# Performance work log

Measured on AMD Instinct MI355X. Metric: run time of the kernel, lower is better.

Reference implementation:

```python
import jax, jax.numpy as jnp
import numpy as np

EPS = 1e-5

def _offset_conv(x, w, b):
    # 3x3 conv, padding=1, producing 2*K*K offset channels (standard DeformConv2D v1)
    out = jax.lax.conv_general_dilated(x, w, (1, 1), ((1, 1), (1, 1)),
                                       dimension_numbers=('NCHW', 'OIHW', 'NCHW'))
    return out + b[None, :, None, None]

def _bilinear_gather(x, py, px):
    # x: [B,C,H,W]; py,px: [B,K2,H,W] float sample coords -> [B,C,K2,H,W]
    B, C, H, W = x.shape
    py = jnp.clip(py, 0.0, H - 1.0)
    px = jnp.clip(px, 0.0, W - 1.0)
    y0 = jnp.floor(py)
    x0 = jnp.floor(px)
    wy = py - y0
    wx = px - x0
    y0i = y0.astype(jnp.int32)
    x0i = x0.astype(jnp.int32)
    y1i = jnp.minimum(y0i + 1, H - 1)
    x1i = jnp.minimum(x0i + 1, W - 1)
    xf = x.reshape(B, C, H * W)
    K2, Ho, Wo = py.shape[1], py.shape[2], py.shape[3]
    def gather(yy, xx):
        idx = (yy * W + xx).reshape(B, 1, -1)  # broadcast over C
        return jnp.take_along_axis(xf, idx, axis=2).reshape(B, C, K2, Ho, Wo)
    v00 = gather(y0i, x0i)
    v01 = gather(y0i, x1i)
    v10 = gather(y1i, x0i)
    v11 = gather(y1i, x1i)
    wy = wy[:, None]
    wx = wx[:, None]
    return (v00 * (1 - wy) * (1 - wx) + v01 * (1 - wy) * wx
            + v10 * wy * (1 - wx) + v11 * wy * wx)

def _deform_dw(x, w_off, b_off, w_dw, k):
    # depthwise deformable conv, kernel k, padding k//2 (same spatial size)
    B, C, H, W = x.shape
    K2 = k * k
    off = _offset_conv(x, w_off, b_off)      # [B, 2*K2, H, W]
    dy, dx = off[:, :K2], off[:, K2:]
    r = (k - 1) // 2
    pn = jnp.arange(-r, r + 1, dtype=x.dtype)
    pn_y = jnp.repeat(pn, k)[None, :, None, None]  # [1,K2,1,1]
    pn_x = jnp.tile(pn, k)[None, :, None, None]
    gy = jnp.arange(H, dtype=x.dtype)[None, None, :, None]
    gx = jnp.arange(W, dtype=x.dtype)[None, None, None, :]
    py = gy + pn_y + dy
    px = gx + pn_x + dx
    samp = _bilinear_gather(x, py, px)        # [B,C,K2,H,W]
    return jnp.einsum('bckhw,ck->bchw', samp, w_dw.reshape(C, K2))

def _bn_relu(x, g, b, m, v):
    inv = g / jnp.sqrt(v + EPS)
    return jax.nn.relu(x * inv[None, :, None, None] + (b - m * inv)[None, :, None, None])

def setup_inputs() -> dict:
    key = jax.random.key(0)
    B, C, H, W, O = 4, 96, 64, 64, 192
    ks = jax.random.split(key, 32)
    d = {'x': jax.random.normal(ks[0], (B, C, H, W), jnp.float32)}
    i = 1
    for k in (3, 5, 7):
        K2 = k * k
        d[f'w_off{k}'] = 0.01 * jax.random.normal(ks[i], (2 * K2, C, 3, 3), jnp.float32); i += 1
        d[f'b_off{k}'] = jnp.zeros((2 * K2,), jnp.float32)
        d[f'w_dw{k}'] = jax.random.normal(ks[i], (C, k, k), jnp.float32) / k; i += 1
        d[f'g{k}'] = jnp.ones((C,), jnp.float32)
        d[f'be{k}'] = jnp.zeros((C,), jnp.float32)
        d[f'm{k}'] = 0.1 * jax.random.normal(ks[i], (C,), jnp.float32); i += 1
        d[f'v{k}'] = jax.random.uniform(ks[i], (C,), jnp.float32, 0.5, 1.5); i += 1
    d['w_pw'] = jax.random.normal(ks[i], (O, 3 * C), jnp.float32) / np.sqrt(3 * C).astype(np.float32); i += 1
    d['gp'] = jnp.ones((O,), jnp.float32)
    d['bp'] = jnp.zeros((O,), jnp.float32)
    d['mp'] = 0.1 * jax.random.normal(ks[i], (O,), jnp.float32); i += 1
    d['vp'] = jax.random.uniform(ks[i], (O,), jnp.float32, 0.5, 1.5)
    return d

def reference(x, w_off3, b_off3, w_dw3, g3, be3, m3, v3,
              w_off5, b_off5, w_dw5, g5, be5, m5, v5,
              w_off7, b_off7, w_dw7, g7, be7, m7, v7,
              w_pw, gp, bp, mp, vp):
    x1 = _bn_relu(_deform_dw(x, w_off3, b_off3, w_dw3, 3), g3, be3, m3, v3)
    x2 = _bn_relu(_deform_dw(x, w_off5, b_off5, w_dw5, 5), g5, be5, m5, v5)
    x3 = _bn_relu(_deform_dw(x, w_off7, b_off7, w_dw7, 7), g7, be7, m7, v7)
    xc = jnp.concatenate([x1, x2, x3], axis=1)  # [B, 3C, H, W]
    out = jnp.einsum('bchw,oc->bohw', xc, w_pw)  # 1x1 conv
    return _bn_relu(out, gp, bp, mp, vp)
```

## Files before the change

kernel.cpp:

```cpp
#include <hip/hip_runtime.h>
#include <hip/hip_fp16.h>
#include <math.h>

typedef unsigned short u16;
typedef _Float16 f16x8 __attribute__((ext_vector_type(8)));
typedef float f32x4 __attribute__((ext_vector_type(4)));

#define HWp 4096
#define Cc 96
#define Bb 4
#define Oo 192
#define C3 288

#define OFF_OFF   0
#define OFF_WDWT  3145728
#define OFF_BCAT  3159840
#define OFF_SBR   3160032
#define OFF_HBR   3160320
#define OFF_SPW   3160608
#define OFF_HPW   3160800
#define FP32_END  3160992
#define BF_XTPAD  0
#define BF_WOF    1672704
#define BF_WPW    1838592
#define BF_YT     1893888

__device__ __forceinline__ u16 f2h(float f) { return __half_as_ushort(__float2half(f)); }
__device__ __forceinline__ unsigned h2u(__half2 h) { union { __half2 h; unsigned u; } t; t.h = h; return t.u; }
__device__ __forceinline__ __half2 u2h(unsigned u) { union { __half2 h; unsigned u; } t; t.u = u; return t.h; }

#define PREP_N (165888 + 55296 + 14112 + 192 + 288 + 288 + 192 + 192 + 24960)
#define PREP_BLK ((PREP_N + 255) / 256)

__global__ __launch_bounds__(256) void prep_kernel(
    const float* __restrict__ x,
    const float* __restrict__ w3, const float* __restrict__ b3, const float* __restrict__ dw3,
    const float* __restrict__ g3, const float* __restrict__ be3, const float* __restrict__ m3, const float* __restrict__ v3,
    const float* __restrict__ w5, const float* __restrict__ b5, const float* __restrict__ dw5,
    const float* __restrict__ g5, const float* __restrict__ be5, const float* __restrict__ m5, const float* __restrict__ v5,
    const float* __restrict__ w7, const float* __restrict__ b7, const float* __restrict__ dw7,
    const float* __restrict__ g7, const float* __restrict__ be7, const float* __restrict__ m7, const float* __restrict__ v7,
    const float* __restrict__ wpw,
    const float* __restrict__ gp, const float* __restrict__ bp, const float* __restrict__ mp, const float* __restrict__ vp,
    float* __restrict__ ws)
{
    __shared__ u16 sT[64 * 104];
    u16* bf = (u16*)(ws + FP32_END);
    const int tid = threadIdx.x;

    if (blockIdx.x < 256) {
        const int b = blockIdx.x >> 6, h = blockIdx.x & 63;
        const float* xb = x + (((size_t)b * Cc) << 12) + (h << 6);
#pragma unroll
        for (int it = 0; it < 24; ++it) {
            int j = tid + it * 256;
            int c = j >> 6, p = j & 63;
            sT[p * 104 + c] = f2h(xb[((size_t)c << 12) + p]);
        }
        __syncthreads();
        u16* dst = bf + BF_XTPAD + ((size_t)(b * 66 + h + 1) * 66 + 1) * 96;
#pragma unroll
        for (int it = 0; it < 6; ++it) {
            int j = tid + it * 256;
            int pos = j / 24, c4 = j % 24;
            const u16* s = &sT[pos * 104 + c4 * 4];
            *(uint2*)(dst + pos * 96 + c4 * 4) = make_uint2(
                (unsigned)s[0] | ((unsigned)s[1] << 16),
                (unsigned)s[2] | ((unsigned)s[3] << 16));
        }
        return;
    }

    int i = (blockIdx.x - 256) * 256 + tid;
    if (i < 165888) {
        int f = i / 13824, r = i % 13824;
        int s = r >> 9, l = r & 511;
        int lane = l >> 3, j = l & 7;
        int o = f * 16 + (lane & 15);
        int k = s * 32 + (lane >> 4) * 8 + j;
        int tap = k / 96, c = k % 96;
        float v = 0.f;
        if (o < 18)       v = w3[o * 864 + c * 9 + tap];
        else if (o < 68)  v = w5[(o - 18) * 864 + c * 9 + tap];
        else if (o < 166) v = w7[(o - 68) * 864 + c * 9 + tap];
        bf[BF_WOF + i] = f2h(v);
        return;
    }
    int j = i - 165888;
    if (j < 55296) {
        int f = j / 4608, r = j % 4608;
        int s = r >> 9, l = r & 511;
        int lane = l >> 3, jj = l & 7;
        int o = f * 16 + (lane & 15);
        int k = s * 32 + (lane >> 4) * 8 + jj;
        bf[BF_WPW + j] = f2h(wpw[o * C3 + k]);
        return;
    }
    j -= 55296;
    if (j < 14112) {
        int ksel = j / 4704, rem = j % 4704;
        int t = rem / 96, c = rem % 96;
        int K2 = (ksel == 0) ? 9 : (ksel == 1) ? 25 : 49;
        const float* dw = (ksel == 0) ? dw3 : (ksel == 1) ? dw5 : dw7;
        ws[OFF_WDWT + j] = (t < K2) ? dw[c * K2 + t] : 0.f;
        return;
    }
    j -= 14112;
    if (j < 192) {
        float v = 0.f;
        if (j < 18)       v = b3[j];
        else if (j < 68)  v = b5[j - 18];
        else if (j < 166) v = b7[j - 68];
        ws[OFF_BCAT + j] = v;
        return;
    }
    j -= 192;
    if (j < C3) {
        int ks = j / Cc, c = j % Cc;
        const float* g = (ks == 0) ? g3 : (ks == 1) ? g5 : g7;
        const float* v = (ks == 0) ? v3 : (ks == 1) ? v5 : v7;
        ws[OFF_SBR + j] = g[c] / sqrtf(v[c] + 1e-5f);
        return;
    }
    j -= C3;
    if (j < C3) {
        int ks = j / Cc, c = j % Cc;
        const float* g = (ks == 0) ? g3 : (ks == 1) ? g5 : g7;
        const float* v = (ks == 0) ? v3 : (ks == 1) ? v5 : v7;
        const float* be = (ks == 0) ? be3 : (ks == 1) ? be5 : be7;
        const float* m = (ks == 0) ? m3 : (ks == 1) ? m5 : m7;
        float inv = g[c] / sqrtf(v[c] + 1e-5f);
        ws[OFF_HBR + j] = be[c] - m[c] * inv;
        return;
    }
    j -= C3;
    if (j < Oo) { ws[OFF_SPW + j] = gp[j] / sqrtf(vp[j] + 1e-5f); return; }
    j -= Oo;
    if (j < Oo) {
        float inv = gp[j] / sqrtf(vp[j] + 1e-5f);
        ws[OFF_HPW + j] = bp[j] - mp[j] * inv;
        return;
    }
    j -= Oo;
    if (j < 24960) {
        int c4 = j % 24, rem = j / 24;
        int cell = rem % 260, bb = rem / 260;
        int row, col;
        if (cell < 66)       { row = 0;  col = cell; }
        else if (cell < 132) { row = 65; col = cell - 66; }
        else if (cell < 196) { row = cell - 132 + 1; col = 0; }
        else                 { row = cell - 196 + 1; col = 65; }
        u16* dst = bf + BF_XTPAD + ((size_t)(bb * 66 + row) * 66 + col) * 96 + c4 * 4;
        *(uint2*)dst = make_uint2(0u, 0u);
        return;
    }
}

__global__ __launch_bounds__(512) void offconv_mfma(
    const float* __restrict__ ws, float* __restrict__ off)
{
    __shared__ u16 sX[3 * 66 * 98];
    const u16* bf = (const u16*)(ws + FP32_END);
    const u16* xp = bf + BF_XTPAD;
    const u16* wof = bf + BF_WOF;
    const int tid = threadIdx.x;
    const int lane = tid & 63, wid = tid >> 6;
    const int lane15 = lane & 15, quad = lane >> 4;
    const int h = blockIdx.x;
    const int b = blockIdx.z;
    const int f0 = (wid >> 2) * 6;
    const int pos = (wid & 3) * 16 + lane15;

#pragma unroll
    for (int it = 0; it < 10; ++it) {
        int j = tid + it * 512;
        if (j < 4752) {
            int r = j / (66 * 24);
            int rem = j % (66 * 24);
            int col = rem / 24, c4 = rem % 24;
            uint2 v = *(const uint2*)(xp + ((size_t)((b * 66 + h + r) * 66 + col)) * 96 + c4 * 4);
            *(uint2*)(&sX[(r * 66 + col) * 98 + c4 * 4]) = v;
        }
    }
    __syncthreads();

    f32x4 acc[6];
#pragma unroll
    for (int f = 0; f < 6; ++f) acc[f] = (f32x4){0.f, 0.f, 0.f, 0.f};

#pragma unroll
    for (int tap = 0; tap < 9; ++tap) {
        const int ky = tap / 3, kx = tap % 3;
        const u16* brow = &sX[(ky * 66 + kx + pos) * 98 + quad * 8];
#pragma unroll
        for (int cc = 0; cc < 3; ++cc) {
            f16x8 bb = *(const f16x8*)(brow + cc * 32);
            const int s = tap * 3 + cc;
#pragma unroll
            for (int f = 0; f < 6; ++f) {
                f16x8 a = *(const f16x8*)(wof + ((size_t)((f0 + f) * 27 + s) * 64 + lane) * 8);
                acc[f] = __builtin_amdgcn_mfma_f32_16x16x32_f16(a, bb, acc[f], 0, 0, 0);
            }
        }
    }

    const float* bcat = ws + OFF_BCAT;
    const int p = (h << 6) + pos;
#pragma unroll
    for (int f = 0; f < 6; ++f) {
        float* dst = off + (((size_t)(b * 192 + (f0 + f) * 16 + quad * 4)) << 12) + p;
#pragma unroll
        for (int r = 0; r < 4; ++r)
            dst[(size_t)r << 12] = acc[f][r] + bcat[(f0 + f) * 16 + quad * 4 + r];
    }
}

template<int K>
__device__ __forceinline__ void samp_v7(
    int ksel, int p0, int rounds, uint4* __restrict__ sWI,
    const float* __restrict__ ws, u16* __restrict__ yt)
{
    constexpr int K2 = K * K;
    constexpr int R = (K - 1) / 2;
    const int tb = (ksel == 0) ? 0 : ((ksel == 1) ? 18 : 68);

    const int tid = threadIdx.x;
    const int b = blockIdx.z;
    const float* offb = ws + OFF_OFF + ((size_t)(b * 192 + tb)) * HWp;
    const int c8 = tid % 12;
    const int q  = tid / 12;
    const int c = c8 * 8;
    const u16* xh = (const u16*)(ws + FP32_END) + BF_XTPAD + (size_t)b * 66 * 66 * 96;
    const char* xcb = (const char*)xh + c * 2;
    const float* wdT = ws + OFF_WDWT + ksel * 4704 + c;

    for (int r = 0; r < rounds; ++r) {
        const int p0r = p0 + r * 20;
        for (int i = tid; i < K2 * 20; i += 256) {
            int t = i / 20, qq = i % 20;
            int p = min(p0r + qq, 4095);
            int hh = p >> 6, wp = p & 63;
            float dy = offb[(size_t)t * HWp + p];
            float dx = offb[(size_t)(K2 + t) * HWp + p];
            int ky = t / K - R, kx = t % K - R;
            float py = fminf(fmaxf((float)(hh + ky) + dy, 0.f), 63.f);
            float px = fminf(fmaxf((float)(wp + kx) + dx, 0.f), 63.f);
            float fy = floorf(py), fx = floorf(px);
            int y0 = (int)fy, x0 = (int)fx;
            float wy = py - fy, wx = px - fx;
            int y1 = min(y0 + 1, 63), x1 = min(x0 + 1, 63);
            float w11 = wy * wx;
            float w10 = wy - w11;
            float w01 = wx - w11;
            float w00 = 1.f - wy - wx + w11;
            unsigned wA = h2u(__floats2half2_rn(w00, w01));
            unsigned wB = h2u(__floats2half2_rn(w10, w11));
            unsigned o00 = (unsigned)((y0 + 1) * 66 + (x0 + 1)) * 192u;
            unsigned d01 = (unsigned)(x1 - x0) * 192u;
            unsigned d10 = (unsigned)(y1 - y0) * 12672u;
            sWI[i] = make_uint4(wA, wB, o00, d01 | (d10 << 16));
        }
        __syncthreads();

        const int p = p0r + q;
        if (tid < 240 && p < 4096) {
            float acc[8];
#pragma unroll
            for (int k = 0; k < 8; ++k) acc[k] = 0.f;

            for (int t = 0; t < K2; ++t) {
                const uint4 e = sWI[t * 20 + q];
                const __half2 wA = u2h(e.x), wB = u2h(e.y);
                const __half2 w00b = __low2half2(wA), w01b = __high2half2(wA);
                const __half2 w10b = __low2half2(wB), w11b = __high2half2(wB);
                const unsigned d01 = e.w & 0xffffu, d10 = e.w >> 16;
                const uint4 u00 = *(const uint4*)(xcb + e.z);
                const uint4 u01 = *(const uint4*)(xcb + e.z + d01);
                const uint4 u10 = *(const uint4*)(xcb + e.z + d10);
                const uint4 u11 = *(const uint4*)(xcb + e.z + d10 + d01);
                const float4 wda = *(const float4*)(wdT + t * 96);
                const float4 wdb = *(const float4*)(wdT + t * 96 + 4);
                const unsigned a00[4] = {u00.x, u00.y, u00.z, u00.w};
                const unsigned a01[4] = {u01.x, u01.y, u01.z, u01.w};
                const unsigned a10[4] = {u10.x, u10.y, u10.z, u10.w};
                const unsigned a11[4] = {u11.x, u11.y, u11.z, u11.w};
                const float wd[8] = {wda.x, wda.y, wda.z, wda.w, wdb.x, wdb.y, wdb.z, wdb.w};
#pragma unroll
                for (int d = 0; d < 4; ++d) {
                    __half2 v = __hmul2(w00b, u2h(a00[d]));
                    v = __hfma2(w01b, u2h(a01[d]), v);
                    v = __hfma2(w10b, u2h(a10[d]), v);
                    v = __hfma2(w11b, u2h(a11[d]), v);
                    acc[2 * d]     = fmaf(wd[2 * d],     __low2float(v),  acc[2 * d]);
                    acc[2 * d + 1] = fmaf(wd[2 * d + 1], __high2float(v), acc[2 * d + 1]);
                }
            }

            const int cb = ksel * Cc + c;
            const float4 sa = *(const float4*)(ws + OFF_SBR + cb);
            const float4 sb = *(const float4*)(ws + OFF_SBR + cb + 4);
            const float4 ha = *(const float4*)(ws + OFF_HBR + cb);
            const float4 hb = *(const float4*)(ws + OFF_HBR + cb + 4);
            const float ss[8] = {sa.x, sa.y, sa.z, sa.w, sb.x, sb.y, sb.z, sb.w};
            const float hh8[8] = {ha.x, ha.y, ha.z, ha.w, hb.x, hb.y, hb.z, hb.w};
            unsigned rr[4];
#pragma unroll
            for (int d = 0; d < 4; ++d) {
                float lo = fmaxf(fmaf(acc[2 * d],     ss[2 * d],     hh8[2 * d]),     0.f);
                float hi = fmaxf(fmaf(acc[2 * d + 1], ss[2 * d + 1], hh8[2 * d + 1]), 0.f);
                rr[d] = h2u(__floats2half2_rn(lo, hi));
            }
            *(uint4*)(yt + ((size_t)(b << 12) + p) * C3 + cb) = make_uint4(rr[0], rr[1], rr[2], rr[3]);
        }
        if (r + 1 < rounds) __syncthreads();
    }
}

__global__ __launch_bounds__(256, 6) void sampdw7_kernel(float* __restrict__ ws)
{
    __shared__ uint4 sWI[980];
    u16* yt = (u16*)(ws + FP32_END) + BF_YT;
    const int bx = blockIdx.x;
    if (bx < 41)        samp_v7<3>(0, bx * 100, 5, sWI, ws, yt);
    else if (bx < 144)  samp_v7<5>(1, (bx - 41) * 40, 2, sWI, ws, yt);
    else                samp_v7<7>(2, (bx - 144) * 20, 1, sWI, ws, yt);
}

__global__ __launch_bounds__(512) void pwconv_mfma(
    const float* __restrict__ ws, float* __restrict__ out)
{
    __shared__ u16 sB[64 * 296];
    const u16* bf = (const u16*)(ws + FP32_END);
    const u16* yt = bf + BF_YT;
    const u16* wpw = bf + BF_WPW;
    const int tid = threadIdx.x;
    const int lane = tid & 63, wid = tid >> 6;
    const int lane15 = lane & 15, quad = lane >> 4;
    const int p0 = blockIdx.x * 64;
    const int b = blockIdx.z;
    const int f0 = (wid >> 2) * 6;
    const int pos = (wid & 3) * 16 + lane15;

#pragma unroll
    for (int it = 0; it < 5; ++it) {
        int j = tid + it * 512;
        if (j < 2304) {
            int ps = j / 36, c8 = j % 36;
            *(uint4*)(&sB[ps * 296 + c8 * 8]) =
                *(const uint4*)(yt + ((size_t)(b << 12) + p0 + ps) * C3 + c8 * 8);
        }
    }
    __syncthreads();

    f32x4 acc[6];
#pragma unroll
    for (int f = 0; f < 6; ++f) acc[f] = (f32x4){0.f, 0.f, 0.f, 0.f};

    const u16* brow = &sB[pos * 296 + quad * 8];
#pragma unroll
    for (int s = 0; s < 9; ++s) {
        f16x8 bb = *(const f16x8*)(brow + s * 32);
#pragma unroll
        for (int f = 0; f < 6; ++f) {
            f16x8 a = *(const f16x8*)(wpw + ((size_t)((f0 + f) * 9 + s) * 64 + lane) * 8);
            acc[f] = __builtin_amdgcn_mfma_f32_16x16x32_f16(a, bb, acc[f], 0, 0, 0);
        }
    }

    const float* spw = ws + OFF_SPW;
    const float* hpw = ws + OFF_HPW;
    const int p = p0 + pos;
#pragma unroll
    for (int f = 0; f < 6; ++f) {
        float* dst = out + (((size_t)(b * Oo + (f0 + f) * 16 + quad * 4)) << 12) + p;
#pragma unroll
        for (int r = 0; r < 4; ++r) {
            int o = (f0 + f) * 16 + quad * 4 + r;
            dst[(size_t)r << 12] = fmaxf(fmaf(acc[f][r], spw[o], hpw[o]), 0.f);
        }
    }
}

extern "C" void kernel_launch(void* const* d_in, const int* in_sizes, int n_in,
                              void* d_out, int out_size, void* d_ws, size_t ws_size,
                              hipStream_t stream)
{
    const float* x     = (const float*)d_in[0];
    const float* w3    = (const float*)d_in[1];
    const float* b3    = (const float*)d_in[2];
    const float* dw3   = (const float*)d_in[3];
    const float* g3    = (const float*)d_in[4];
    const float* be3   = (const float*)d_in[5];
    const float* m3    = (const float*)d_in[6];
    const float* v3    = (const float*)d_in[7];
    const float* w5    = (const float*)d_in[8];
    const float* b5    = (const float*)d_in[9];
    const float* dw5   = (const float*)d_in[10];
    const float* g5    = (const float*)d_in[11];
    const float* be5   = (const float*)d_in[12];
    const float* m5    = (const float*)d_in[13];
    const float* v5    = (const float*)d_in[14];
    const float* w7    = (const float*)d_in[15];
    const float* b7    = (const float*)d_in[16];
    const float* dw7   = (const float*)d_in[17];
    const float* g7    = (const float*)d_in[18];
    const float* be7   = (const float*)d_in[19];
    const float* m7    = (const float*)d_in[20];
    const float* v7    = (const float*)d_in[21];
    const float* wpw   = (const float*)d_in[22];
    const float* gp    = (const float*)d_in[23];
    const float* bp    = (const float*)d_in[24];
    const float* mp    = (const float*)d_in[25];
    const float* vp    = (const float*)d_in[26];

    float* ws = (float*)d_ws;
    float* out = (float*)d_out;

    {
        prep_kernel<<<256 + PREP_BLK, 256, 0, stream>>>(
            x,
            w3, b3, dw3, g3, be3, m3, v3,
            w5, b5, dw5, g5, be5, m5, v5,
            w7, b7, dw7, g7, be7, m7, v7,
            wpw, gp, bp, mp, vp, ws);
    }
    {
        dim3 grid(64, 1, Bb);
        offconv_mfma<<<grid, 512, 0, stream>>>(ws, ws + OFF_OFF);
    }
    {
        dim3 grid(349, 1, Bb);
        sampdw7_kernel<<<grid, 256, 0, stream>>>(ws);
    }
    {
        dim3 grid(64, 1, Bb);
        pwconv_mfma<<<grid, 512, 0, stream>>>(ws, out);
    }
}
```

Before: 191.0 us.

## Fuse offset conv, deformable sampling and pointwise conv into one kernel

Replaces the three kernels (offset conv, deformable depthwise sampling, pointwise conv) with a single kernel that processes 16-pixel tiles. Offsets and the per-tile sampled activations stay in shared memory instead of being written to and re-read from global workspace. This removes two launches and the global traffic for the offset and intermediate tensors. In exchange, each block repeats the weight loads for a small tile, and only 192 of 256 threads are active during sampling, which may reduce parallelism per block.

```diff
diff --git a/kernel.cpp b/kernel.cpp
--- a/kernel.cpp
+++ b/kernel.cpp
@@ -12,18 +12,16 @@
 #define Oo 192
 #define C3 288
 
-#define OFF_OFF   0
-#define OFF_WDWT  3145728
-#define OFF_BCAT  3159840
-#define OFF_SBR   3160032
-#define OFF_HBR   3160320
-#define OFF_SPW   3160608
-#define OFF_HPW   3160800
-#define FP32_END  3160992
+#define OFF_WDWT  0
+#define OFF_BCAT  14112
+#define OFF_SBR   14304
+#define OFF_HBR   14592
+#define OFF_SPW   14880
+#define OFF_HPW   15072
+#define FP32_END  15264
 #define BF_XTPAD  0
 #define BF_WOF    1672704
 #define BF_WPW    1838592
-#define BF_YT     1893888
 
 __device__ __forceinline__ u16 f2h(float f) { return __half_as_ushort(__float2half(f)); }
 __device__ __forceinline__ unsigned h2u(__half2 h) { union { __half2 h; unsigned u; } t; t.h = h; return t.u; }
@@ -156,130 +154,127 @@
     }
 }
 
-__global__ __launch_bounds__(512) void offconv_mfma(
-    const float* __restrict__ ws, float* __restrict__ off)
+__global__ __launch_bounds__(256, 4) void mega_kernel(
+    const float* __restrict__ ws, float* __restrict__ out)
 {
-    __shared__ u16 sX[3 * 66 * 98];
+    __shared__ uint4 regA[1328];
+    __shared__ float regB[3072];
+    u16* sX = (u16*)regA;
+    uint4* sWI = regA;
+    float* soff = regB;
+    u16* ytile = (u16*)regB;
+
     const u16* bf = (const u16*)(ws + FP32_END);
     const u16* xp = bf + BF_XTPAD;
-    const u16* wof = bf + BF_WOF;
     const int tid = threadIdx.x;
     const int lane = tid & 63, wid = tid >> 6;
     const int lane15 = lane & 15, quad = lane >> 4;
-    const int h = blockIdx.x;
     const int b = blockIdx.z;
-    const int f0 = (wid >> 2) * 6;
-    const int pos = (wid & 3) * 16 + lane15;
-
-#pragma unroll
-    for (int it = 0; it < 10; ++it) {
-        int j = tid + it * 512;
-        if (j < 4752) {
-            int r = j / (66 * 24);
-            int rem = j % (66 * 24);
+    const int p0 = blockIdx.x * 16;
+    const int h = p0 >> 6;
+    const int w0 = p0 & 63;
+
+    {
+        const u16* src = xp + ((size_t)(b * 66 + h) * 66 + w0) * 96;
+        for (int j = tid; j < 1296; j += 256) {
+            int r = j / 432;
+            int rem = j % 432;
             int col = rem / 24, c4 = rem % 24;
-            uint2 v = *(const uint2*)(xp + ((size_t)((b * 66 + h + r) * 66 + col)) * 96 + c4 * 4);
-            *(uint2*)(&sX[(r * 66 + col) * 98 + c4 * 4]) = v;
+            uint2 v = *(const uint2*)(src + ((size_t)(r * 66 + col)) * 96 + c4 * 4);
+            *(uint2*)(&sX[(r * 18 + col) * 104 + c4 * 4]) = v;
         }
     }
     __syncthreads();
 
-    f32x4 acc[6];
-#pragma unroll
-    for (int f = 0; f < 6; ++f) acc[f] = (f32x4){0.f, 0.f, 0.f, 0.f};
-
-#pragma unroll
-    for (int tap = 0; tap < 9; ++tap) {
-        const int ky = tap / 3, kx = tap % 3;
-        const u16* brow = &sX[(ky * 66 + kx + pos) * 98 + quad * 8];
-#pragma unroll
-        for (int cc = 0; cc < 3; ++cc) {
-            f16x8 bb = *(const f16x8*)(brow + cc * 32);
-            const int s = tap * 3 + cc;
-#pragma unroll
-            for (int f = 0; f < 6; ++f) {
-                f16x8 a = *(const f16x8*)(wof + ((size_t)((f0 + f) * 27 + s) * 64 + lane) * 8);
-                acc[f] = __builtin_amdgcn_mfma_f32_16x16x32_f16(a, bb, acc[f], 0, 0, 0);
-            }
-        }
-    }
-
-    const float* bcat = ws + OFF_BCAT;
-    const int p = (h << 6) + pos;
-#pragma unroll
-    for (int f = 0; f < 6; ++f) {
-        float* dst = off + (((size_t)(b * 192 + (f0 + f) * 16 + quad * 4)) << 12) + p;
-#pragma unroll
-        for (int r = 0; r < 4; ++r)
-            dst[(size_t)r << 12] = acc[f][r] + bcat[(f0 + f) * 16 + quad * 4 + r];
-    }
-}
-
-template<int K>
-__device__ __forceinline__ void samp_v7(
-    int ksel, int p0, int rounds, uint4* __restrict__ sWI,
-    const float* __restrict__ ws, u16* __restrict__ yt)
-{
-    constexpr int K2 = K * K;
-    constexpr int R = (K - 1) / 2;
-    const int tb = (ksel == 0) ? 0 : ((ksel == 1) ? 18 : 68);
-
-    const int tid = threadIdx.x;
-    const int b = blockIdx.z;
-    const float* offb = ws + OFF_OFF + ((size_t)(b * 192 + tb)) * HWp;
-    const int c8 = tid % 12;
-    const int q  = tid / 12;
-    const int c = c8 * 8;
-    const u16* xh = (const u16*)(ws + FP32_END) + BF_XTPAD + (size_t)b * 66 * 66 * 96;
-    const char* xcb = (const char*)xh + c * 2;
-    const float* wdT = ws + OFF_WDWT + ksel * 4704 + c;
-
-    for (int r = 0; r < rounds; ++r) {
-        const int p0r = p0 + r * 20;
-        for (int i = tid; i < K2 * 20; i += 256) {
-            int t = i / 20, qq = i % 20;
-            int p = min(p0r + qq, 4095);
-            int hh = p >> 6, wp = p & 63;
-            float dy = offb[(size_t)t * HWp + p];
-            float dx = offb[(size_t)(K2 + t) * HWp + p];
-            int ky = t / K - R, kx = t % K - R;
-            float py = fminf(fmaxf((float)(hh + ky) + dy, 0.f), 63.f);
-            float px = fminf(fmaxf((float)(wp + kx) + dx, 0.f), 63.f);
-            float fy = floorf(py), fx = floorf(px);
-            int y0 = (int)fy, x0 = (int)fx;
-            float wy = py - fy, wx = px - fx;
-            int y1 = min(y0 + 1, 63), x1 = min(x0 + 1, 63);
-            float w11 = wy * wx;
-            float w10 = wy - w11;
-            float w01 = wx - w11;
-            float w00 = 1.f - wy - wx + w11;
-            unsigned wA = h2u(__floats2half2_rn(w00, w01));
-            unsigned wB = h2u(__floats2half2_rn(w10, w11));
-            unsigned o00 = (unsigned)((y0 + 1) * 66 + (x0 + 1)) * 192u;
-            unsigned d01 = (unsigned)(x1 - x0) * 192u;
-            unsigned d10 = (unsigned)(y1 - y0) * 12672u;
-            sWI[i] = make_uint4(wA, wB, o00, d01 | (d10 << 16));
-        }
-        __syncthreads();
-
-        const int p = p0r + q;
-        if (tid < 240 && p < 4096) {
+    {
+        const u16* wof = bf + BF_WOF;
+        f32x4 acc[3];
+#pragma unroll
+        for (int ff = 0; ff < 3; ++ff) acc[ff] = (f32x4){0.f, 0.f, 0.f, 0.f};
+#pragma unroll
+        for (int tap = 0; tap < 9; ++tap) {
+            const int ky2 = tap / 3, kx2 = tap % 3;
+            const u16* brow = &sX[(ky2 * 18 + kx2 + lane15) * 104 + quad * 8];
+#pragma unroll
+            for (int cc = 0; cc < 3; ++cc) {
+                f16x8 bb = *(const f16x8*)(brow + cc * 32);
+                const int s = tap * 3 + cc;
+#pragma unroll
+                for (int ff = 0; ff < 3; ++ff) {
+                    const int f = wid * 3 + ff;
+                    f16x8 a = *(const f16x8*)(wof + ((size_t)(f * 27 + s) * 64 + lane) * 8);
+                    acc[ff] = __builtin_amdgcn_mfma_f32_16x16x32_f16(a, bb, acc[ff], 0, 0, 0);
+                }
+            }
+        }
+        const float* bcat = ws + OFF_BCAT;
+#pragma unroll
+        for (int ff = 0; ff < 3; ++ff) {
+#pragma unroll
+            for (int r = 0; r < 4; ++r) {
+                int co = (wid * 3 + ff) * 16 + quad * 4 + r;
+                soff[co * 16 + lane15] = acc[ff][r] + bcat[co];
+            }
+        }
+    }
+    __syncthreads();
+
+    for (int i = tid; i < 1328; i += 256) {
+        int gt = i >> 4, q = i & 15;
+        int K, K2, R, tb, t;
+        if (gt < 9)       { K = 3; K2 = 9;  R = 1; tb = 0;  t = gt; }
+        else if (gt < 34) { K = 5; K2 = 25; R = 2; tb = 18; t = gt - 9; }
+        else              { K = 7; K2 = 49; R = 3; tb = 68; t = gt - 34; }
+        int ky = t / K - R, kx = t % K - R;
+        float dy = soff[(tb + t) * 16 + q];
+        float dx = soff[(tb + K2 + t) * 16 + q];
+        float py = fminf(fmaxf((float)(h + ky) + dy, 0.f), 63.f);
+        float px = fminf(fmaxf((float)(w0 + q + kx) + dx, 0.f), 63.f);
+        float fy = floorf(py), fx = floorf(px);
+        int y0 = (int)fy, x0 = (int)fx;
+        float wy = py - fy, wx = px - fx;
+        int y1 = min(y0 + 1, 63), x1 = min(x0 + 1, 63);
+        float w11 = wy * wx;
+        float w10 = wy - w11;
+        float w01 = wx - w11;
+        float w00 = 1.f - wy - wx + w11;
+        unsigned wA = h2u(__floats2half2_rn(w00, w01));
+        unsigned wB = h2u(__floats2half2_rn(w10, w11));
+        unsigned o00 = (unsigned)((y0 + 1) * 66 + (x0 + 1)) * 192u;
+        unsigned d01 = (unsigned)(x1 - x0) * 192u;
+        unsigned d10 = (unsigned)(y1 - y0) * 12672u;
+        sWI[i] = make_uint4(wA, wB, o00, d01 | (d10 << 16));
+    }
+    __syncthreads();
+
+    if (tid < 192) {
+        const int c8 = tid % 12;
+        const int q  = tid / 12;
+        const int c = c8 * 8;
+        const u16* xh = xp + (size_t)b * 66 * 66 * 96;
+        const char* xcb = (const char*)xh + c * 2;
+
+#pragma unroll
+        for (int seg = 0; seg < 3; ++seg) {
+            const int g0 = (seg == 0) ? 0 : (seg == 1) ? 9 : 34;
+            const int g1 = (seg == 0) ? 9 : (seg == 1) ? 34 : 83;
+            const float* wdT = ws + OFF_WDWT + seg * 4704 + c;
             float acc[8];
 #pragma unroll
             for (int k = 0; k < 8; ++k) acc[k] = 0.f;
 
-            for (int t = 0; t < K2; ++t) {
-                const uint4 e = sWI[t * 20 + q];
-                const __half2 wA = u2h(e.x), wB = u2h(e.y);
-                const __half2 w00b = __low2half2(wA), w01b = __high2half2(wA);
-                const __half2 w10b = __low2half2(wB), w11b = __high2half2(wB);
+            for (int gt = g0; gt < g1; ++gt) {
+                const uint4 e = sWI[(gt << 4) + q];
+                const __half2 wAh = u2h(e.x), wBh = u2h(e.y);
+                const __half2 w00b = __low2half2(wAh), w01b = __high2half2(wAh);
+                const __half2 w10b = __low2half2(wBh), w11b = __high2half2(wBh);
                 const unsigned d01 = e.w & 0xffffu, d10 = e.w >> 16;
                 const uint4 u00 = *(const uint4*)(xcb + e.z);
                 const uint4 u01 = *(const uint4*)(xcb + e.z + d01);
                 const uint4 u10 = *(const uint4*)(xcb + e.z + d10);
                 const uint4 u11 = *(const uint4*)(xcb + e.z + d10 + d01);
-                const float4 wda = *(const float4*)(wdT + t * 96);
-                const float4 wdb = *(const float4*)(wdT + t * 96 + 4);
+                const float4 wda = *(const float4*)(wdT + (gt - g0) * 96);
+                const float4 wdb = *(const float4*)(wdT + (gt - g0) * 96 + 4);
                 const unsigned a00[4] = {u00.x, u00.y, u00.z, u00.w};
                 const unsigned a01[4] = {u01.x, u01.y, u01.z, u01.w};
                 const unsigned a10[4] = {u10.x, u10.y, u10.z, u10.w};
@@ -296,7 +291,7 @@
                 }
             }
 
-            const int cb = ksel * Cc + c;
+            const int cb = seg * Cc + c;
             const float4 sa = *(const float4*)(ws + OFF_SBR + cb);
             const float4 sb = *(const float4*)(ws + OFF_SBR + cb + 4);
             const float4 ha = *(const float4*)(ws + OFF_HBR + cb);
@@ -310,73 +305,38 @@
                 float hi = fmaxf(fmaf(acc[2 * d + 1], ss[2 * d + 1], hh8[2 * d + 1]), 0.f);
                 rr[d] = h2u(__floats2half2_rn(lo, hi));
             }
-            *(uint4*)(yt + ((size_t)(b << 12) + p) * C3 + cb) = make_uint4(rr[0], rr[1], rr[2], rr[3]);
-        }
-        if (r + 1 < rounds) __syncthreads();
-    }
-}
-
-__global__ __launch_bounds__(256, 6) void sampdw7_kernel(float* __restrict__ ws)
-{
-    __shared__ uint4 sWI[980];
-    u16* yt = (u16*)(ws + FP32_END) + BF_YT;
-    const int bx = blockIdx.x;
-    if (bx < 41)        samp_v7<3>(0, bx * 100, 5, sWI, ws, yt);
-    else if (bx < 144)  samp_v7<5>(1, (bx - 41) * 40, 2, sWI, ws, yt);
-    else                samp_v7<7>(2, (bx - 144) * 20, 1, sWI, ws, yt);
-}
-
-__global__ __launch_bounds__(512) void pwconv_mfma(
-    const float* __restrict__ ws, float* __restrict__ out)
-{
-    __shared__ u16 sB[64 * 296];
-    const u16* bf = (const u16*)(ws + FP32_END);
-    const u16* yt = bf + BF_YT;
-    const u16* wpw = bf + BF_WPW;
-    const int tid = threadIdx.x;
-    const int lane = tid & 63, wid = tid >> 6;
-    const int lane15 = lane & 15, quad = lane >> 4;
-    const int p0 = blockIdx.x * 64;
-    const int b = blockIdx.z;
-    const int f0 = (wid >> 2) * 6;
-    const int pos = (wid & 3) * 16 + lane15;
-
-#pragma unroll
-    for (int it = 0; it < 5; ++it) {
-        int j = tid + it * 512;
-        if (j < 2304) {
-            int ps = j / 36, c8 = j % 36;
-            *(uint4*)(&sB[ps * 296 + c8 * 8]) =
-                *(const uint4*)(yt + ((size_t)(b << 12) + p0 + ps) * C3 + c8 * 8);
+            *(uint4*)(ytile + q * 296 + cb) = make_uint4(rr[0], rr[1], rr[2], rr[3]);
         }
     }
     __syncthreads();
 
-    f32x4 acc[6];
-#pragma unroll
-    for (int f = 0; f < 6; ++f) acc[f] = (f32x4){0.f, 0.f, 0.f, 0.f};
-
-    const u16* brow = &sB[pos * 296 + quad * 8];
-#pragma unroll
-    for (int s = 0; s < 9; ++s) {
-        f16x8 bb = *(const f16x8*)(brow + s * 32);
-#pragma unroll
-        for (int f = 0; f < 6; ++f) {
-            f16x8 a = *(const f16x8*)(wpw + ((size_t)((f0 + f) * 9 + s) * 64 + lane) * 8);
-            acc[f] = __builtin_amdgcn_mfma_f32_16x16x32_f16(a, bb, acc[f], 0, 0, 0);
-        }
-    }
-
-    const float* spw = ws + OFF_SPW;
-    const float* hpw = ws + OFF_HPW;
-    const int p = p0 + pos;
-#pragma unroll
-    for (int f = 0; f < 6; ++f) {
-        float* dst = out + (((size_t)(b * Oo + (f0 + f) * 16 + quad * 4)) << 12) + p;
-#pragma unroll
-        for (int r = 0; r < 4; ++r) {
-            int o = (f0 + f) * 16 + quad * 4 + r;
-            dst[(size_t)r << 12] = fmaxf(fmaf(acc[f][r], spw[o], hpw[o]), 0.f);
+    {
+        const u16* wpw = bf + BF_WPW;
+        f32x4 acc[3];
+#pragma unroll
+        for (int ff = 0; ff < 3; ++ff) acc[ff] = (f32x4){0.f, 0.f, 0.f, 0.f};
+        const u16* brow = &ytile[lane15 * 296 + quad * 8];
+#pragma unroll
+        for (int s = 0; s < 9; ++s) {
+            f16x8 bb = *(const f16x8*)(brow + s * 32);
+#pragma unroll
+            for (int ff = 0; ff < 3; ++ff) {
+                const int f = wid * 3 + ff;
+                f16x8 a = *(const f16x8*)(wpw + ((size_t)(f * 9 + s) * 64 + lane) * 8);
+                acc[ff] = __builtin_amdgcn_mfma_f32_16x16x32_f16(a, bb, acc[ff], 0, 0, 0);
+            }
+        }
+        const float* spw = ws + OFF_SPW;
+        const float* hpw = ws + OFF_HPW;
+        const int p = p0 + lane15;
+#pragma unroll
+        for (int ff = 0; ff < 3; ++ff) {
+#pragma unroll
+            for (int r = 0; r < 4; ++r) {
+                int o = (wid * 3 + ff) * 16 + quad * 4 + r;
+                out[(((size_t)(b * Oo + o)) << 12) + p] =
+                    fmaxf(fmaf(acc[ff][r], spw[o], hpw[o]), 0.f);
+            }
         }
     }
 }
@@ -425,15 +385,7 @@
             wpw, gp, bp, mp, vp, ws);
     }
     {
-        dim3 grid(64, 1, Bb);
-        offconv_mfma<<<grid, 512, 0, stream>>>(ws, ws + OFF_OFF);
-    }
-    {
-        dim3 grid(349, 1, Bb);
-        sampdw7_kernel<<<grid, 256, 0, stream>>>(ws);
-    }
-    {
-        dim3 grid(64, 1, Bb);
-        pwconv_mfma<<<grid, 512, 0, stream>>>(ws, out);
+        dim3 grid(256, 1, Bb);
+        mega_kernel<<<grid, 256, 0, stream>>>(ws, out);
     }
 }
```

Measured after the change: 176.9 us. 1.08x faster.
